# Optimization experiments

Measured on AMD Instinct MI355X. Metric: run time of the kernel, lower is better.

Reference implementation:

```python
import jax, jax.numpy as jnp
import numpy as np

D = 1024
H = 16
HD = D // H
E = 64
K = 2


def setup_inputs() -> dict:
    key = jax.random.key(0)
    ks = jax.random.split(key, 10)
    s = 0.02
    return {
        "x": jax.random.normal(ks[0], (8, 2048, D), dtype=jnp.float32),
        "expert_embeddings": jax.random.normal(ks[1], (E, D), dtype=jnp.float32),
        "in_proj_w": jax.random.normal(ks[2], (3 * D, D), dtype=jnp.float32) * s,
        "in_proj_b": jax.random.normal(ks[3], (3 * D,), dtype=jnp.float32) * s,
        "out_proj_w": jax.random.normal(ks[4], (D, D), dtype=jnp.float32) * s,
        "out_proj_b": jax.random.normal(ks[5], (D,), dtype=jnp.float32) * s,
        "gate_w1": jax.random.normal(ks[6], (4 * E, D), dtype=jnp.float32) * s,
        "gate_b1": jax.random.normal(ks[7], (4 * E,), dtype=jnp.float32) * s,
        "gate_w2": jax.random.normal(ks[8], (E, 4 * E), dtype=jnp.float32) * s,
        "gate_b2": jax.random.normal(ks[9], (E,), dtype=jnp.float32) * s,
    }


def reference(x, expert_embeddings, in_proj_w, in_proj_b, out_proj_w, out_proj_b,
              gate_w1, gate_b1, gate_w2, gate_b2):
    B, S, _ = x.shape
    wq, wk, wv = jnp.split(in_proj_w, 3, axis=0)   # each (D, D)
    bq, bk, bv = jnp.split(in_proj_b, 3, axis=0)
    # cross-attention: queries from x, keys/values from expert embeddings (shared across batch)
    q = (x @ wq.T + bq).reshape(B, S, H, HD)                      # (B,S,H,hd)
    k = (expert_embeddings @ wk.T + bk).reshape(E, H, HD)         # (E,H,hd)
    v = (expert_embeddings @ wv.T + bv).reshape(E, H, HD)
    scores = jnp.einsum('bshd,ehd->bhse', q, k) / jnp.sqrt(jnp.float32(HD))
    attn = jax.nn.softmax(scores, axis=-1)                        # (B,H,S,E)
    o = jnp.einsum('bhse,ehd->bshd', attn, v).reshape(B, S, D)
    attn_out = o @ out_proj_w.T + out_proj_b                      # (B,S,D)
    # gate MLP (exact GELU like torch default)
    h = jax.nn.gelu(attn_out @ gate_w1.T + gate_b1, approximate=False)
    gate_logits = h @ gate_w2.T + gate_b2                         # (B,S,E)
    probs = jax.nn.softmax(gate_logits, axis=-1)
    vals, idx = jax.lax.top_k(probs, K)                           # (B,S,K)
    weights = vals / (jnp.sum(vals, axis=-1, keepdims=True) + 1e-8)
    return idx, weights
```

## Files before the change

### kernel.cpp

```cpp
#include <hip/hip_runtime.h>
#include <math.h>


typedef _Float16 h8 __attribute__((ext_vector_type(8)));
typedef _Float16 h4 __attribute__((ext_vector_type(4)));
typedef float f4 __attribute__((ext_vector_type(4)));

#define SWZ(row, slot) ((row) * 32 + ((((slot) ^ ((row) & 3))) * 8))

__device__ __forceinline__ float gelu_exact(float x) {
    return 0.5f * x * (1.0f + erff(x * 0.70710678118654752f));
}

__global__ __launch_bounds__(256) void split2_kernel(
    const float* __restrict__ src, _Float16* __restrict__ dst, long total, int colsh) {
    long i = ((long)blockIdx.x * 256 + threadIdx.x) * 4;
    if (i >= total) return;
    f4 v = *(const f4*)(src + i);
    long row = i >> colsh; int col = (int)(i & ((1 << colsh) - 1));
    _Float16* d0 = dst + (row << (colsh + 1)) + col;
    h4 lo, hi;
    #pragma unroll
    for (int j = 0; j < 4; j++) {
        _Float16 a = (_Float16)v[j];
        lo[j] = a;
        hi[j] = (_Float16)((v[j] - (float)a) * 4096.0f);
    }
    *(h4*)d0 = lo;
    *(h4*)(d0 + (1 << colsh)) = hi;
}

__global__ __launch_bounds__(256) void kv_kernel(
    const float* __restrict__ w, const float* __restrict__ b,
    const float* __restrict__ ee, float* __restrict__ kbuf, float* __restrict__ vtbuf) {
    __shared__ float As[32][68];
    __shared__ float Bs[32][68];
    int tid = threadIdx.x;
    int r0 = blockIdx.x * 64;
    int tx = tid & 15, ty = tid >> 4;
    float acc[4][4] = {};
    const float* wbase = w + (size_t)(1024 + r0) * 1024;
    for (int k0 = 0; k0 < 1024; k0 += 32) {
        #pragma unroll
        for (int i = 0; i < 2; i++) {
            int f = tid + i * 256;
            int row = f >> 3, c4 = f & 7;
            float4 v = *(const float4*)(wbase + (size_t)row * 1024 + k0 + c4 * 4);
            As[c4*4+0][row] = v.x; As[c4*4+1][row] = v.y;
            As[c4*4+2][row] = v.z; As[c4*4+3][row] = v.w;
            float4 u = *(const float4*)(ee + (size_t)row * 1024 + k0 + c4 * 4);
            Bs[c4*4+0][row] = u.x; Bs[c4*4+1][row] = u.y;
            Bs[c4*4+2][row] = u.z; Bs[c4*4+3][row] = u.w;
        }
        __syncthreads();
        #pragma unroll
        for (int kk = 0; kk < 32; kk++) {
            float a[4], bb[4];
            *(float4*)&a[0]  = *(const float4*)&As[kk][ty * 4];
            *(float4*)&bb[0] = *(const float4*)&Bs[kk][tx * 4];
            #pragma unroll
            for (int i = 0; i < 4; i++)
                #pragma unroll
                for (int j = 0; j < 4; j++)
                    acc[i][j] = fmaf(a[i], bb[j], acc[i][j]);
        }
        __syncthreads();
    }
    #pragma unroll
    for (int i = 0; i < 4; i++) {
        int row = r0 + ty * 4 + i;
        float bias = b[1024 + row];
        int j = row & 1023;
        int h = j >> 6, hd = j & 63;
        #pragma unroll
        for (int jj = 0; jj < 4; jj++) {
            int e = tx * 4 + jj;
            float val = acc[i][jj] + bias;
            if (row < 1024) kbuf[h * 4096 + e * 64 + hd] = val;
            else            vtbuf[h * 4096 + hd * 64 + e] = val;
        }
    }
}

template<int GELU, int OSPLIT>
__global__ __launch_bounds__(256, 2) void hgemm_kernel(
    const _Float16* __restrict__ A, const _Float16* __restrict__ B,
    const float* __restrict__ bias, void* __restrict__ Cv, int ldc, int nhalf) {
    __shared__ __align__(16) _Float16 As[128 * 32];
    __shared__ __align__(16) _Float16 Bl[128 * 32];
    __shared__ __align__(16) _Float16 Bh[128 * 32];
    int tid = threadIdx.x;
    int m0 = blockIdx.y * 128, n0 = blockIdx.x * 128;
    int w = tid >> 6, l = tid & 63;
    int wm = w & 1, wn = w >> 1;
    int lr = l & 15, lk = l >> 4;

    f4 acc1[4][4], acc2[4][4];
    #pragma unroll
    for (int i = 0; i < 4; i++)
        #pragma unroll
        for (int j = 0; j < 4; j++) {
            acc1[i][j] = (f4){0.f, 0.f, 0.f, 0.f};
            acc2[i][j] = (f4){0.f, 0.f, 0.f, 0.f};
        }

    int f0 = tid, f1 = tid + 256;
    int r0 = f0 >> 2, c0 = f0 & 3, r1 = f1 >> 2, c1 = f1 & 3;
    int s0 = SWZ(r0, c0), s1 = SWZ(r1, c1);
    const _Float16* Ab = A + (size_t)m0 * 2048;
    const _Float16* Bb = B + (size_t)n0 * 2048;

    uint4 ua0, ua1, ub0, ub1, uc0, uc1;
    ua0 = *(const uint4*)(Ab + (size_t)r0 * 2048 + c0 * 8);
    ua1 = *(const uint4*)(Ab + (size_t)r1 * 2048 + c1 * 8);
    ub0 = *(const uint4*)(Bb + (size_t)r0 * 2048 + c0 * 8);
    ub1 = *(const uint4*)(Bb + (size_t)r1 * 2048 + c1 * 8);
    uc0 = *(const uint4*)(Bb + (size_t)r0 * 2048 + 1024 + c0 * 8);
    uc1 = *(const uint4*)(Bb + (size_t)r1 * 2048 + 1024 + c1 * 8);

    for (int kt = 0; kt < 32; kt++) {
        __syncthreads();
        *(uint4*)(As + s0) = ua0; *(uint4*)(As + s1) = ua1;
        *(uint4*)(Bl + s0) = ub0; *(uint4*)(Bl + s1) = ub1;
        *(uint4*)(Bh + s0) = uc0; *(uint4*)(Bh + s1) = uc1;
        __syncthreads();
        if (kt < 31) {
            int ka = (kt + 1) * 32;
            ua0 = *(const uint4*)(Ab + (size_t)r0 * 2048 + ka + c0 * 8);
            ua1 = *(const uint4*)(Ab + (size_t)r1 * 2048 + ka + c1 * 8);
            ub0 = *(const uint4*)(Bb + (size_t)r0 * 2048 + ka + c0 * 8);
            ub1 = *(const uint4*)(Bb + (size_t)r1 * 2048 + ka + c1 * 8);
            uc0 = *(const uint4*)(Bb + (size_t)r0 * 2048 + 1024 + ka + c0 * 8);
            uc1 = *(const uint4*)(Bb + (size_t)r1 * 2048 + 1024 + ka + c1 * 8);
        } else {
            ua0 = *(const uint4*)(Ab + (size_t)r0 * 2048 + 1024 + c0 * 8);
            ua1 = *(const uint4*)(Ab + (size_t)r1 * 2048 + 1024 + c1 * 8);
            uc0 = *(const uint4*)(Bb + (size_t)r0 * 2048 + c0 * 8);
            uc1 = *(const uint4*)(Bb + (size_t)r1 * 2048 + c1 * 8);
        }
        h8 af[4], blf[4], bhf[4];
        #pragma unroll
        for (int mi = 0; mi < 4; mi++)
            af[mi] = *(const h8*)(As + SWZ(wm * 64 + mi * 16 + lr, lk));
        #pragma unroll
        for (int ni = 0; ni < 4; ni++) {
            blf[ni] = *(const h8*)(Bl + SWZ(wn * 64 + ni * 16 + lr, lk));
            bhf[ni] = *(const h8*)(Bh + SWZ(wn * 64 + ni * 16 + lr, lk));
        }
        #pragma unroll
        for (int mi = 0; mi < 4; mi++)
            #pragma unroll
            for (int ni = 0; ni < 4; ni++) {
                acc1[mi][ni] = __builtin_amdgcn_mfma_f32_16x16x32_f16(af[mi], blf[ni], acc1[mi][ni], 0, 0, 0);
                acc2[mi][ni] = __builtin_amdgcn_mfma_f32_16x16x32_f16(af[mi], bhf[ni], acc2[mi][ni], 0, 0, 0);
            }
    }

    for (int kt = 0; kt < 32; kt++) {
        __syncthreads();
        *(uint4*)(As + s0) = ua0; *(uint4*)(As + s1) = ua1;
        *(uint4*)(Bh + s0) = uc0; *(uint4*)(Bh + s1) = uc1;
        __syncthreads();
        if (kt < 31) {
            int ka = (kt + 1) * 32;
            ua0 = *(const uint4*)(Ab + (size_t)r0 * 2048 + 1024 + ka + c0 * 8);
            ua1 = *(const uint4*)(Ab + (size_t)r1 * 2048 + 1024 + ka + c1 * 8);
            uc0 = *(const uint4*)(Bb + (size_t)r0 * 2048 + ka + c0 * 8);
            uc1 = *(const uint4*)(Bb + (size_t)r1 * 2048 + ka + c1 * 8);
        }
        h8 af[4], bhf[4];
        #pragma unroll
        for (int mi = 0; mi < 4; mi++)
            af[mi] = *(const h8*)(As + SWZ(wm * 64 + mi * 16 + lr, lk));
        #pragma unroll
        for (int ni = 0; ni < 4; ni++)
            bhf[ni] = *(const h8*)(Bh + SWZ(wn * 64 + ni * 16 + lr, lk));
        #pragma unroll
        for (int mi = 0; mi < 4; mi++)
            #pragma unroll
            for (int ni = 0; ni < 4; ni++)
                acc2[mi][ni] = __builtin_amdgcn_mfma_f32_16x16x32_f16(af[mi], bhf[ni], acc2[mi][ni], 0, 0, 0);
    }

    #pragma unroll
    for (int mi = 0; mi < 4; mi++)
        #pragma unroll
        for (int ni = 0; ni < 4; ni++) {
            int n = n0 + wn * 64 + ni * 16 + lr;
            float bn = bias[n];
            #pragma unroll
            for (int j = 0; j < 4; j++) {
                int m = m0 + wm * 64 + mi * 16 + lk * 4 + j;
                float val = acc1[mi][ni][j] + acc2[mi][ni][j] * (1.0f / 4096.0f) + bn;
                if (GELU) val = gelu_exact(val);
                if (OSPLIT) {
                    _Float16* Ch = (_Float16*)Cv;
                    _Float16 lo = (_Float16)val;
                    Ch[(size_t)m * ldc + n] = lo;
                    Ch[(size_t)m * ldc + nhalf + n] = (_Float16)((val - (float)lo) * 4096.0f);
                } else {
                    ((float*)Cv)[(size_t)m * ldc + n] = val;
                }
            }
        }
}

__global__ __launch_bounds__(256) void attn2_kernel(
    const float* __restrict__ kbuf, const float* __restrict__ vtbuf,
    const float* __restrict__ q, _Float16* __restrict__ os) {
    __shared__ __align__(16) float qs[4][64][68];
    __shared__ __align__(16) float ps[4][2][64];
    int tid = threadIdx.x;
    int w = tid >> 6, l = tid & 63;
    int wid = blockIdx.x * 4 + w;
    int b = wid >> 9, h = (wid >> 5) & 15, t0 = (wid & 31) * 64;

    f4 kr[16], vt[16];
    const f4* kp = (const f4*)(kbuf + h * 4096 + l * 64);
    const f4* vp = (const f4*)(vtbuf + h * 4096 + l * 64);
    #pragma unroll
    for (int i = 0; i < 16; i++) { kr[i] = kp[i]; vt[i] = vp[i]; }

    const float* qbase = q + ((size_t)(b * 2048 + t0)) * 1024 + h * 64;
    #pragma unroll
    for (int it = 0; it < 16; it++) {
        int f = it * 64 + l;
        int r = f >> 4, c = f & 15;
        f4 v = *(const f4*)(qbase + (size_t)r * 1024 + c * 4);
        *(f4*)&qs[w][r][c * 4] = v;
    }

    for (int t = 0; t < 64; t++) {
        float s = 0.f;
        #pragma unroll
        for (int i = 0; i < 16; i++) {
            f4 qv = *(const f4*)&qs[w][t][i * 4];
            s = fmaf(qv[0], kr[i][0], s);
            s = fmaf(qv[1], kr[i][1], s);
            s = fmaf(qv[2], kr[i][2], s);
            s = fmaf(qv[3], kr[i][3], s);
        }
        s *= 0.125f;
        float ex = __expf(s);
        float sum = ex;
        #pragma unroll
        for (int off = 32; off; off >>= 1) sum += __shfl_xor(sum, off, 64);
        float p = ex / sum;
        ps[w][t & 1][l] = p;
        float o = 0.f;
        #pragma unroll
        for (int i = 0; i < 16; i++) {
            f4 pv = *(const f4*)&ps[w][t & 1][i * 4];
            o = fmaf(pv[0], vt[i][0], o);
            o = fmaf(pv[1], vt[i][1], o);
            o = fmaf(pv[2], vt[i][2], o);
            o = fmaf(pv[3], vt[i][3], o);
        }
        _Float16 o1 = (_Float16)o;
        _Float16 o2 = (_Float16)((o - (float)o1) * 4096.0f);
        size_t tok = (size_t)(b * 2048 + t0 + t);
        os[tok * 2048 + h * 64 + l] = o1;
        os[tok * 2048 + 1024 + h * 64 + l] = o2;
    }
}

__global__ __launch_bounds__(256) void gate2_kernel(
    const _Float16* __restrict__ h1s, const _Float16* __restrict__ w2s,
    const float* __restrict__ b2, float* __restrict__ out) {
    int tid = threadIdx.x;
    int w = tid >> 6, l = tid & 63;
    int lr = l & 15, lk = l >> 4;
    int trow = blockIdx.x * 64 + w * 16;

    f4 acc1[4], acc2[4], acc3[4];
    #pragma unroll
    for (int ni = 0; ni < 4; ni++) {
        acc1[ni] = (f4){0.f,0.f,0.f,0.f};
        acc2[ni] = (f4){0.f,0.f,0.f,0.f};
        acc3[ni] = (f4){0.f,0.f,0.f,0.f};
    }
    const _Float16* Arow = h1s + (size_t)(trow + lr) * 512;
    #pragma unroll
    for (int kt = 0; kt < 8; kt++) {
        h8 a1 = *(const h8*)(Arow + kt * 32 + lk * 8);
        h8 a2 = *(const h8*)(Arow + 256 + kt * 32 + lk * 8);
        #pragma unroll
        for (int ni = 0; ni < 4; ni++) {
            const _Float16* Brow = w2s + (size_t)(ni * 16 + lr) * 512;
            h8 b1 = *(const h8*)(Brow + kt * 32 + lk * 8);
            h8 bh = *(const h8*)(Brow + 256 + kt * 32 + lk * 8);
            acc1[ni] = __builtin_amdgcn_mfma_f32_16x16x32_f16(a1, b1, acc1[ni], 0, 0, 0);
            acc2[ni] = __builtin_amdgcn_mfma_f32_16x16x32_f16(a1, bh, acc2[ni], 0, 0, 0);
            acc2[ni] = __builtin_amdgcn_mfma_f32_16x16x32_f16(a2, b1, acc2[ni], 0, 0, 0);
            acc3[ni] = __builtin_amdgcn_mfma_f32_16x16x32_f16(a2, bh, acc3[ni], 0, 0, 0);
        }
    }
    float bcol[4];
    #pragma unroll
    for (int ni = 0; ni < 4; ni++) bcol[ni] = b2[ni * 16 + lr];

    const float c1 = 1.0f / 4096.0f, c2 = 1.0f / 16777216.0f;
    #pragma unroll
    for (int j = 0; j < 4; j++) {
        int tok = trow + lk * 4 + j;
        float lg[4];
        #pragma unroll
        for (int ni = 0; ni < 4; ni++)
            lg[ni] = acc1[ni][j] + acc2[ni][j] * c1 + acc3[ni][j] * c2 + bcol[ni];
        float mx = fmaxf(fmaxf(lg[0], lg[1]), fmaxf(lg[2], lg[3]));
        #pragma unroll
        for (int off = 1; off <= 8; off <<= 1) mx = fmaxf(mx, __shfl_xor(mx, off, 64));
        float pr[4], s = 0.f;
        #pragma unroll
        for (int ni = 0; ni < 4; ni++) { pr[ni] = expf(lg[ni] - mx); s += pr[ni]; }
        #pragma unroll
        for (int off = 1; off <= 8; off <<= 1) s += __shfl_xor(s, off, 64);
        float inv = 1.0f / s;
        float v1 = -1.f, v2 = -1.f; int i1 = 0, i2 = 0;
        #pragma unroll
        for (int ni = 0; ni < 4; ni++) {
            float p = pr[ni] * inv;
            int e = ni * 16 + lr;
            if (p > v1) { v2 = v1; i2 = i1; v1 = p; i1 = e; }
            else if (p > v2) { v2 = p; i2 = e; }
        }
        #pragma unroll
        for (int off = 1; off <= 8; off <<= 1) {
            float u1 = __shfl_xor(v1, off, 64); int k1 = __shfl_xor(i1, off, 64);
            float u2 = __shfl_xor(v2, off, 64); int k2 = __shfl_xor(i2, off, 64);
            if (u1 > v1) {
                if (v1 > u2) { v2 = v1; i2 = i1; } else { v2 = u2; i2 = k2; }
                v1 = u1; i1 = k1;
            } else if (u1 > v2) { v2 = u1; i2 = k1; }
        }
        if (lr == 0) {
            float wsum = v1 + v2 + 1e-8f;
            out[(size_t)tok * 2]     = (float)i1;
            out[(size_t)tok * 2 + 1] = (float)i2;
            out[32768 + (size_t)tok * 2]     = v1 / wsum;
            out[32768 + (size_t)tok * 2 + 1] = v2 / wsum;
        }
    }
}

extern "C" void kernel_launch(void* const* d_in, const int* in_sizes, int n_in,
                              void* d_out, int out_size, void* d_ws, size_t ws_size,
                              hipStream_t stream) {
    const float* x   = (const float*)d_in[0];
    const float* ee  = (const float*)d_in[1];
    const float* ipw = (const float*)d_in[2];
    const float* ipb = (const float*)d_in[3];
    const float* opw = (const float*)d_in[4];
    const float* opb = (const float*)d_in[5];
    const float* gw1 = (const float*)d_in[6];
    const float* gb1 = (const float*)d_in[7];
    const float* gw2 = (const float*)d_in[8];
    const float* gb2 = (const float*)d_in[9];
    float* out = (float*)d_out;
    char* ws = (char*)d_ws;

    _Float16* xs    = (_Float16*)ws;
    _Float16* h1s   = (_Float16*)ws;
    float*    qbuf  = (float*)(ws + 67108864);
    _Float16* aos   = (_Float16*)(ws + 67108864);
    _Float16* wqs   = (_Float16*)(ws + 134217728);
    _Float16* opws  = (_Float16*)(ws + 138412032);
    _Float16* gw1s  = (_Float16*)(ws + 142606336);
    float*    kbuf  = (float*)(ws + 143654912);
    _Float16* gw2s  = (_Float16*)(ws + 143654912);
    float*    vtbuf = (float*)(ws + 143917056);

    split2_kernel<<<dim3(1024),  dim3(256), 0, stream>>>(ipw, wqs, 1048576L, 10);
    split2_kernel<<<dim3(1024),  dim3(256), 0, stream>>>(opw, opws, 1048576L, 10);
    split2_kernel<<<dim3(256),   dim3(256), 0, stream>>>(gw1, gw1s, 262144L, 10);
    split2_kernel<<<dim3(16384), dim3(256), 0, stream>>>(x, xs, 16777216L, 10);
    kv_kernel<<<dim3(32), dim3(256), 0, stream>>>(ipw, ipb, ee, kbuf, vtbuf);
    hgemm_kernel<0,0><<<dim3(8, 128), dim3(256), 0, stream>>>(xs, wqs, ipb, qbuf, 1024, 0);
    attn2_kernel<<<dim3(1024), dim3(256), 0, stream>>>(kbuf, vtbuf, qbuf, xs);
    split2_kernel<<<dim3(16), dim3(256), 0, stream>>>(gw2, gw2s, 16384L, 8);
    hgemm_kernel<0,1><<<dim3(8, 128), dim3(256), 0, stream>>>(xs, opws, opb, (void*)aos, 2048, 1024);
    hgemm_kernel<1,1><<<dim3(2, 128), dim3(256), 0, stream>>>(aos, gw1s, gb1, (void*)h1s, 512, 256);
    gate2_kernel<<<dim3(256), dim3(256), 0, stream>>>(h1s, gw2s, gb2, out);
}
```

Before: 630.5 us.

## Fuse x fp16 split into Q GEMM, single-pass split-precision loop, XCD-aware block remap

The separate split kernel that turned x into hi/lo fp16 halves is removed. The Q projection GEMM now reads fp32 x directly and does the split while staging into shared memory, which drops a large write and read-back of a 64MB intermediate. The two-pass K loop (lo*B, then hi*B) becomes one pass that loads the A lo/hi tiles and the B lo/hi tiles together and issues three MFMA groups per tile. Workgroup IDs are also remapped in strides of 8, likely to improve L2 locality across chiplets. In exchange the LDS XOR swizzle is dropped, which may bring back bank conflicts, and LDS use grows by one tile.

```diff
diff --git a/kernel.cpp b/kernel.cpp
--- a/kernel.cpp
+++ b/kernel.cpp
@@ -5,8 +5,6 @@
 typedef _Float16 h8 __attribute__((ext_vector_type(8)));
 typedef _Float16 h4 __attribute__((ext_vector_type(4)));
 typedef float f4 __attribute__((ext_vector_type(4)));
-
-#define SWZ(row, slot) ((row) * 32 + ((((slot) ^ ((row) & 3))) * 8))
 
 __device__ __forceinline__ float gelu_exact(float x) {
     return 0.5f * x * (1.0f + erff(x * 0.70710678118654752f));
@@ -82,15 +80,22 @@
     }
 }
 
-template<int GELU, int OSPLIT>
+template<int GELU, int OSPLIT, int AF32>
 __global__ __launch_bounds__(256, 2) void hgemm_kernel(
-    const _Float16* __restrict__ A, const _Float16* __restrict__ B,
+    const void* __restrict__ Av, const _Float16* __restrict__ B,
     const float* __restrict__ bias, void* __restrict__ Cv, int ldc, int nhalf) {
     __shared__ __align__(16) _Float16 As[128 * 32];
+    __shared__ __align__(16) _Float16 Ah[128 * 32];
     __shared__ __align__(16) _Float16 Bl[128 * 32];
     __shared__ __align__(16) _Float16 Bh[128 * 32];
     int tid = threadIdx.x;
-    int m0 = blockIdx.y * 128, n0 = blockIdx.x * 128;
+
+    int gx = gridDim.x;
+    int nwg = gx * gridDim.y;
+    int lid = blockIdx.y * gx + blockIdx.x;
+    int L = (lid & 7) * (nwg >> 3) + (lid >> 3);
+    int m0 = (L / gx) * 128, n0 = (L % gx) * 128;
+
     int w = tid >> 6, l = tid & 63;
     int wm = w & 1, wn = w >> 1;
     int lr = l & 15, lk = l >> 4;
@@ -104,82 +109,96 @@
             acc2[i][j] = (f4){0.f, 0.f, 0.f, 0.f};
         }
 
-    int f0 = tid, f1 = tid + 256;
-    int r0 = f0 >> 2, c0 = f0 & 3, r1 = f1 >> 2, c1 = f1 & 3;
-    int s0 = SWZ(r0, c0), s1 = SWZ(r1, c1);
-    const _Float16* Ab = A + (size_t)m0 * 2048;
+    int r0 = tid >> 2, c0 = tid & 3;
+    int s0 = r0 * 32 + c0 * 8, s1 = s0 + 64 * 32;
+    int rb = tid >> 3, c4 = tid & 7;
+
+    const _Float16* Ab = (const _Float16*)Av + (size_t)m0 * 2048;
+    const float*    Af = (const float*)Av + (size_t)m0 * 1024;
     const _Float16* Bb = B + (size_t)n0 * 2048;
 
-    uint4 ua0, ua1, ub0, ub1, uc0, uc1;
-    ua0 = *(const uint4*)(Ab + (size_t)r0 * 2048 + c0 * 8);
-    ua1 = *(const uint4*)(Ab + (size_t)r1 * 2048 + c1 * 8);
+    float4 xa[4];
+    uint4 ua0, ua1, uh0, uh1, ub0, ub1, uc0, uc1;
+    if (AF32) {
+        #pragma unroll
+        for (int f = 0; f < 4; f++)
+            xa[f] = *(const float4*)(Af + (size_t)(rb + f * 32) * 1024 + c4 * 4);
+    } else {
+        ua0 = *(const uint4*)(Ab + (size_t)r0 * 2048 + c0 * 8);
+        ua1 = *(const uint4*)(Ab + (size_t)(r0 + 64) * 2048 + c0 * 8);
+        uh0 = *(const uint4*)(Ab + (size_t)r0 * 2048 + 1024 + c0 * 8);
+        uh1 = *(const uint4*)(Ab + (size_t)(r0 + 64) * 2048 + 1024 + c0 * 8);
+    }
     ub0 = *(const uint4*)(Bb + (size_t)r0 * 2048 + c0 * 8);
-    ub1 = *(const uint4*)(Bb + (size_t)r1 * 2048 + c1 * 8);
+    ub1 = *(const uint4*)(Bb + (size_t)(r0 + 64) * 2048 + c0 * 8);
     uc0 = *(const uint4*)(Bb + (size_t)r0 * 2048 + 1024 + c0 * 8);
-    uc1 = *(const uint4*)(Bb + (size_t)r1 * 2048 + 1024 + c1 * 8);
+    uc1 = *(const uint4*)(Bb + (size_t)(r0 + 64) * 2048 + 1024 + c0 * 8);
 
     for (int kt = 0; kt < 32; kt++) {
         __syncthreads();
-        *(uint4*)(As + s0) = ua0; *(uint4*)(As + s1) = ua1;
+        if (AF32) {
+            #pragma unroll
+            for (int f = 0; f < 4; f++) {
+                h4 lo, hi;
+                #pragma unroll
+                for (int j = 0; j < 4; j++) {
+                    float v = ((const float*)&xa[f])[j];
+                    _Float16 a = (_Float16)v;
+                    lo[j] = a;
+                    hi[j] = (_Float16)((v - (float)a) * 4096.0f);
+                }
+                *(h4*)(As + (rb + f * 32) * 32 + c4 * 4) = lo;
+                *(h4*)(Ah + (rb + f * 32) * 32 + c4 * 4) = hi;
+            }
+        } else {
+            *(uint4*)(As + s0) = ua0; *(uint4*)(As + s1) = ua1;
+            *(uint4*)(Ah + s0) = uh0; *(uint4*)(Ah + s1) = uh1;
+        }
         *(uint4*)(Bl + s0) = ub0; *(uint4*)(Bl + s1) = ub1;
         *(uint4*)(Bh + s0) = uc0; *(uint4*)(Bh + s1) = uc1;
         __syncthreads();
         if (kt < 31) {
             int ka = (kt + 1) * 32;
-            ua0 = *(const uint4*)(Ab + (size_t)r0 * 2048 + ka + c0 * 8);
-            ua1 = *(const uint4*)(Ab + (size_t)r1 * 2048 + ka + c1 * 8);
+            if (AF32) {
+                #pragma unroll
+                for (int f = 0; f < 4; f++)
+                    xa[f] = *(const float4*)(Af + (size_t)(rb + f * 32) * 1024 + ka + c4 * 4);
+            } else {
+                ua0 = *(const uint4*)(Ab + (size_t)r0 * 2048 + ka + c0 * 8);
+                ua1 = *(const uint4*)(Ab + (size_t)(r0 + 64) * 2048 + ka + c0 * 8);
+                uh0 = *(const uint4*)(Ab + (size_t)r0 * 2048 + 1024 + ka + c0 * 8);
+                uh1 = *(const uint4*)(Ab + (size_t)(r0 + 64) * 2048 + 1024 + ka + c0 * 8);
+            }
             ub0 = *(const uint4*)(Bb + (size_t)r0 * 2048 + ka + c0 * 8);
-            ub1 = *(const uint4*)(Bb + (size_t)r1 * 2048 + ka + c1 * 8);
+            ub1 = *(const uint4*)(Bb + (size_t)(r0 + 64) * 2048 + ka + c0 * 8);
             uc0 = *(const uint4*)(Bb + (size_t)r0 * 2048 + 1024 + ka + c0 * 8);
-            uc1 = *(const uint4*)(Bb + (size_t)r1 * 2048 + 1024 + ka + c1 * 8);
-        } else {
-            ua0 = *(const uint4*)(Ab + (size_t)r0 * 2048 + 1024 + c0 * 8);
-            ua1 = *(const uint4*)(Ab + (size_t)r1 * 2048 + 1024 + c1 * 8);
-            uc0 = *(const uint4*)(Bb + (size_t)r0 * 2048 + c0 * 8);
-            uc1 = *(const uint4*)(Bb + (size_t)r1 * 2048 + c1 * 8);
-        }
-        h8 af[4], blf[4], bhf[4];
+            uc1 = *(const uint4*)(Bb + (size_t)(r0 + 64) * 2048 + 1024 + ka + c0 * 8);
+        }
+        h8 a1f[4], blf[4], bhf[4];
         #pragma unroll
         for (int mi = 0; mi < 4; mi++)
-            af[mi] = *(const h8*)(As + SWZ(wm * 64 + mi * 16 + lr, lk));
+            a1f[mi] = *(const h8*)(As + (wm * 64 + mi * 16 + lr) * 32 + lk * 8);
         #pragma unroll
         for (int ni = 0; ni < 4; ni++) {
-            blf[ni] = *(const h8*)(Bl + SWZ(wn * 64 + ni * 16 + lr, lk));
-            bhf[ni] = *(const h8*)(Bh + SWZ(wn * 64 + ni * 16 + lr, lk));
+            blf[ni] = *(const h8*)(Bl + (wn * 64 + ni * 16 + lr) * 32 + lk * 8);
+            bhf[ni] = *(const h8*)(Bh + (wn * 64 + ni * 16 + lr) * 32 + lk * 8);
         }
         #pragma unroll
         for (int mi = 0; mi < 4; mi++)
             #pragma unroll
             for (int ni = 0; ni < 4; ni++) {
-                acc1[mi][ni] = __builtin_amdgcn_mfma_f32_16x16x32_f16(af[mi], blf[ni], acc1[mi][ni], 0, 0, 0);
-                acc2[mi][ni] = __builtin_amdgcn_mfma_f32_16x16x32_f16(af[mi], bhf[ni], acc2[mi][ni], 0, 0, 0);
+                acc1[mi][ni] = __builtin_amdgcn_mfma_f32_16x16x32_f16(a1f[mi], blf[ni], acc1[mi][ni], 0, 0, 0);
+                acc2[mi][ni] = __builtin_amdgcn_mfma_f32_16x16x32_f16(a1f[mi], bhf[ni], acc2[mi][ni], 0, 0, 0);
             }
-    }
-
-    for (int kt = 0; kt < 32; kt++) {
-        __syncthreads();
-        *(uint4*)(As + s0) = ua0; *(uint4*)(As + s1) = ua1;
-        *(uint4*)(Bh + s0) = uc0; *(uint4*)(Bh + s1) = uc1;
-        __syncthreads();
-        if (kt < 31) {
-            int ka = (kt + 1) * 32;
-            ua0 = *(const uint4*)(Ab + (size_t)r0 * 2048 + 1024 + ka + c0 * 8);
-            ua1 = *(const uint4*)(Ab + (size_t)r1 * 2048 + 1024 + ka + c1 * 8);
-            uc0 = *(const uint4*)(Bb + (size_t)r0 * 2048 + ka + c0 * 8);
-            uc1 = *(const uint4*)(Bb + (size_t)r1 * 2048 + ka + c1 * 8);
-        }
-        h8 af[4], bhf[4];
+        h8 a2f[4];
         #pragma unroll
         for (int mi = 0; mi < 4; mi++)
-            af[mi] = *(const h8*)(As + SWZ(wm * 64 + mi * 16 + lr, lk));
-        #pragma unroll
-        for (int ni = 0; ni < 4; ni++)
-            bhf[ni] = *(const h8*)(Bh + SWZ(wn * 64 + ni * 16 + lr, lk));
+            a2f[mi] = *(const h8*)(Ah + (wm * 64 + mi * 16 + lr) * 32 + lk * 8);
         #pragma unroll
         for (int mi = 0; mi < 4; mi++)
             #pragma unroll
             for (int ni = 0; ni < 4; ni++)
-                acc2[mi][ni] = __builtin_amdgcn_mfma_f32_16x16x32_f16(af[mi], bhf[ni], acc2[mi][ni], 0, 0, 0);
+                acc2[mi][ni] = __builtin_amdgcn_mfma_f32_16x16x32_f16(a2f[mi], blf[ni], acc2[mi][ni], 0, 0, 0);
     }
 
     #pragma unroll
@@ -359,7 +378,7 @@
     float* out = (float*)d_out;
     char* ws = (char*)d_ws;
 
-    _Float16* xs    = (_Float16*)ws;
+    _Float16* os    = (_Float16*)ws;
     _Float16* h1s   = (_Float16*)ws;
     float*    qbuf  = (float*)(ws + 67108864);
     _Float16* aos   = (_Float16*)(ws + 67108864);
@@ -370,15 +389,14 @@
     _Float16* gw2s  = (_Float16*)(ws + 143654912);
     float*    vtbuf = (float*)(ws + 143917056);
 
-    split2_kernel<<<dim3(1024),  dim3(256), 0, stream>>>(ipw, wqs, 1048576L, 10);
-    split2_kernel<<<dim3(1024),  dim3(256), 0, stream>>>(opw, opws, 1048576L, 10);
-    split2_kernel<<<dim3(256),   dim3(256), 0, stream>>>(gw1, gw1s, 262144L, 10);
-    split2_kernel<<<dim3(16384), dim3(256), 0, stream>>>(x, xs, 16777216L, 10);
+    split2_kernel<<<dim3(1024), dim3(256), 0, stream>>>(ipw, wqs, 1048576L, 10);
+    split2_kernel<<<dim3(1024), dim3(256), 0, stream>>>(opw, opws, 1048576L, 10);
+    split2_kernel<<<dim3(256),  dim3(256), 0, stream>>>(gw1, gw1s, 262144L, 10);
     kv_kernel<<<dim3(32), dim3(256), 0, stream>>>(ipw, ipb, ee, kbuf, vtbuf);
-    hgemm_kernel<0,0><<<dim3(8, 128), dim3(256), 0, stream>>>(xs, wqs, ipb, qbuf, 1024, 0);
-    attn2_kernel<<<dim3(1024), dim3(256), 0, stream>>>(kbuf, vtbuf, qbuf, xs);
+    hgemm_kernel<0,0,1><<<dim3(8, 128), dim3(256), 0, stream>>>(x, wqs, ipb, qbuf, 1024, 0);
+    attn2_kernel<<<dim3(1024), dim3(256), 0, stream>>>(kbuf, vtbuf, qbuf, os);
     split2_kernel<<<dim3(16), dim3(256), 0, stream>>>(gw2, gw2s, 16384L, 8);
-    hgemm_kernel<0,1><<<dim3(8, 128), dim3(256), 0, stream>>>(xs, opws, opb, (void*)aos, 2048, 1024);
-    hgemm_kernel<1,1><<<dim3(2, 128), dim3(256), 0, stream>>>(aos, gw1s, gb1, (void*)h1s, 512, 256);
+    hgemm_kernel<0,1,0><<<dim3(8, 128), dim3(256), 0, stream>>>(os, opws, opb, (void*)aos, 2048, 1024);
+    hgemm_kernel<1,1,0><<<dim3(2, 128), dim3(256), 0, stream>>>(aos, gw1s, gb1, (void*)h1s, 512, 256);
     gate2_kernel<<<dim3(256), dim3(256), 0, stream>>>(h1s, gw2s, gb2, out);
 }
```

Measured after the change: 570.5 us. -9.5%, faster.
